# Kernel optimization log

Hardware: AMD Instinct MI355X
Metric: run time of the kernel (lower is better)

The kernel has to match this reference:

```python
import jax, jax.numpy as jnp
import numpy as np

N_JOINTS = 18

_RELATIVE_JOINT_MAP = np.array([[0,3,2,1,3,3,3,3,3,3,3,3,3,3,3,3,3,3],[3,0,2,3,1,1,3,3,3,3,2,3,2,2,2,3,3,3],[2,2,0,1,1,3,3,3,1,2,2,3,3,3,3,3,3,3],[1,3,1,0,2,3,3,3,2,3,3,3,3,3,3,3,3,3],[3,1,1,2,0,2,3,2,2,3,1,3,3,3,3,3,3,3],[3,1,3,3,2,0,3,3,3,3,3,3,1,1,1,3,3,3],[3,3,3,3,3,3,0,3,2,1,3,3,3,3,3,3,3,3],[3,3,3,3,2,3,3,0,2,3,1,1,3,3,3,2,2,2],[3,3,1,2,2,3,2,2,0,1,1,3,3,3,3,3,3,3],[3,3,2,3,3,3,1,3,1,0,2,3,3,3,3,3,3,3],[3,2,2,3,1,3,3,1,1,2,0,2,3,3,3,3,3,3],[3,3,3,3,3,3,3,1,3,3,2,0,3,3,3,1,1,1],[3,2,3,3,3,1,3,3,3,3,3,3,0,1,2,3,3,3],[3,2,3,3,3,1,3,3,3,3,3,3,1,0,2,3,3,3],[3,2,3,3,3,1,3,3,3,3,3,3,2,2,0,3,3,3],[3,3,3,3,3,3,3,2,3,3,3,1,3,3,3,0,1,2],[3,3,3,3,3,3,3,2,3,3,3,1,3,3,3,1,0,2],[3,3,3,3,3,3,3,2,3,3,3,1,3,3,3,2,2,0]], dtype=np.int32)

DIM = 512
HEADS = 8
DEPTH = DIM // HEADS  # 64
BATCH = 4096


def setup_inputs() -> dict:
    key = jax.random.key(0)
    ks = jax.random.split(key, 10)
    std = 0.02
    return {
        "k": jax.random.normal(ks[0], (BATCH, N_JOINTS, DIM), jnp.float32),
        "v": jax.random.normal(ks[1], (BATCH, N_JOINTS, DIM), jnp.float32),
        "q": jax.random.normal(ks[2], (BATCH, N_JOINTS, DIM), jnp.float32),
        "Wq": jax.random.normal(ks[3], (DIM, DIM), jnp.float32) * (DIM ** -0.5),
        "Wk": jax.random.normal(ks[4], (DIM, DIM), jnp.float32) * (DIM ** -0.5),
        "Wv": jax.random.normal(ks[5], (DIM, DIM), jnp.float32) * (DIM ** -0.5),
        "Wo": jax.random.normal(ks[6], (DIM, DIM), jnp.float32) * (DIM ** -0.5),
        "bo": jnp.zeros((DIM,), jnp.float32),
        "rel_k": jax.random.normal(ks[7], (4, DEPTH), jnp.float32) * std,
        "rel_v": jax.random.normal(ks[8], (4, DEPTH), jnp.float32) * std,
        "joint_map": jnp.asarray(_RELATIVE_JOINT_MAP),
    }


def reference(k, v, q, Wq, Wk, Wv, Wo, bo, rel_k, rel_v, joint_map):
    B, n, dim = q.shape
    h, d = HEADS, DEPTH
    scale = d ** -0.5

    def split_heads(x):  # [B, n, h*d] -> [B, h, n, d]
        return x.reshape(B, n, h, d).transpose(0, 2, 1, 3)

    qh = split_heads(q @ Wq)
    kh = split_heads(k @ Wk)
    vh = split_heads(v @ Wv)

    # gather relative position tables: [n, n, d]
    r_pos_k = rel_k[joint_map]
    r_pos_v = rel_v[joint_map]

    # relative bias sums over heads AND depth of K (faithful to original einsum)
    rel_bias = jnp.einsum('bhid,ijd->bij', kh, r_pos_k)  # [B, n, n]
    dots = (jnp.einsum('bhid,bhjd->bhij', qh, kh) + rel_bias[:, None, :, :]) * scale
    att = jax.nn.softmax(dots, axis=-1)  # [B, h, n, n]

    out = jnp.einsum('bhij,bhjd->bhid', att, vh) + jnp.einsum('bhij,ijd->bhid', att, r_pos_v)
    out = out.transpose(0, 2, 1, 3).reshape(B, n, dim)
    out = out @ Wo + bo
    return out, att
```

## Files before the change

kernel.cpp:

```cpp
#include <hip/hip_runtime.h>
#include <stdint.h>

#define BATCH 4096
#define NJ 18
#define DIMM 512
#define HEADS 8
#define DEPTH 64
#define MROWS (BATCH*NJ)
#define ATT_OFF ((size_t)MROWS*DIMM)

typedef float f32x4 __attribute__((ext_vector_type(4)));
typedef _Float16 f16_t;
typedef _Float16 f16x8 __attribute__((ext_vector_type(8)));

__device__ __forceinline__ void gl_lds16(const unsigned int* g, unsigned int* l) {
    __builtin_amdgcn_global_load_lds(g, l, 16, 0, 0);
}

__global__ __launch_bounds__(256) void convert_w_kernel(
    const float* __restrict__ W0, const float* __restrict__ W1,
    const float* __restrict__ W2, const float* __restrict__ W3,
    f16_t* __restrict__ T0, f16_t* __restrict__ T1,
    f16_t* __restrict__ T2, f16_t* __restrict__ T3)
{
    const float* W = blockIdx.z == 0 ? W0 : blockIdx.z == 1 ? W1 : blockIdx.z == 2 ? W2 : W3;
    f16_t* T       = blockIdx.z == 0 ? T0 : blockIdx.z == 1 ? T1 : blockIdx.z == 2 ? T2 : T3;
    __shared__ float ld[64][65];
    int k0 = blockIdx.y * 64, n0 = blockIdx.x * 64;
    int tid = threadIdx.x;
    #pragma unroll
    for (int it = 0; it < 16; ++it) {
        int idx = tid + it * 256;
        int kk = idx >> 6, nn = idx & 63;
        ld[kk][nn] = W[(size_t)(k0 + kk) * DIMM + n0 + nn];
    }
    __syncthreads();
    f16x8* T8 = (f16x8*)T;
    #pragma unroll
    for (int it = 0; it < 2; ++it) {
        int c = tid + it * 256;
        int nn = c >> 3, c8 = c & 7;
        int n = n0 + nn, k = k0 + c8 * 8;
        f16x8 val;
        #pragma unroll
        for (int e = 0; e < 8; ++e) val[e] = (f16_t)ld[c8 * 8 + e][nn];
        size_t vi = (size_t)((n >> 7) * 8 + (k >> 6)) * 1024
                  + (n & 127) * 8 + (((k >> 3) & 7) ^ (n & 7));
        T8[vi] = val;
    }
}

template <int MODE>
__global__ __launch_bounds__(256) void gemm16_kernel(
    const void* __restrict__ A0, const void* __restrict__ A1,
    const void* __restrict__ A2,
    const f16_t* __restrict__ B0, const f16_t* __restrict__ B1,
    const f16_t* __restrict__ B2,
    void* __restrict__ C0, void* __restrict__ C1, void* __restrict__ C2,
    const float* __restrict__ bias)
{
    const void* Aparm = blockIdx.z == 0 ? A0 : blockIdx.z == 1 ? A1 : A2;
    const f16_t* Bt   = blockIdx.z == 0 ? B0 : blockIdx.z == 1 ? B1 : B2;
    void* Cparm       = blockIdx.z == 0 ? C0 : blockIdx.z == 1 ? C1 : C2;

    const int p = blockIdx.x + 4 * blockIdx.y;
    const int logical = (p & 7) * (2304 / 8) + (p >> 3);
    const int bn = (logical & 3) * 128;
    const int bm = (logical >> 2) * 128;

    __shared__ __align__(16) f16_t As[128 * 64];
    __shared__ __align__(16) f16_t Bs[128 * 64];

    const int tid = threadIdx.x;
    const int lane = tid & 63;
    const int wv = tid >> 6;
    const int wm = wv >> 1, wn = wv & 1;
    const int l15 = lane & 15, lg = lane >> 4;
    const int swz = (l15 & 7) << 4;
    const int koffb[2] = { (lg * 16) ^ swz, (lg * 16 + 64) ^ swz };

    f32x4 acc[4][4] = {};

    for (int ks = 0; ks < 8; ++ks) {
        __syncthreads();
        {
            const unsigned int* btile =
                (const unsigned int*)(Bt + (size_t)((bn >> 7) * 8 + ks) * 8192);
            unsigned int* bs = (unsigned int*)Bs;
            #pragma unroll
            for (int it = 0; it < 4; ++it) {
                int chunk = wv * 4 + it;
                gl_lds16(btile + chunk * 256 + lane * 4, bs + chunk * 256);
            }
        }
        if constexpr (MODE == 0) {
            const float* A = (const float*)Aparm;
            #pragma unroll
            for (int r = 0; r < 4; ++r) {
                int c = tid + r * 256;
                int row = c >> 3, kc = c & 7;
                const f32x4* p4 = (const f32x4*)(A + (size_t)(bm + row) * DIMM + ks * 64 + kc * 8);
                f32x4 a0 = p4[0], a1 = p4[1];
                f16x8 val;
                val[0] = (f16_t)a0[0]; val[1] = (f16_t)a0[1];
                val[2] = (f16_t)a0[2]; val[3] = (f16_t)a0[3];
                val[4] = (f16_t)a1[0]; val[5] = (f16_t)a1[1];
                val[6] = (f16_t)a1[2]; val[7] = (f16_t)a1[3];
                ((f16x8*)As)[row * 8 + (kc ^ (row & 7))] = val;
            }
        } else {
            const unsigned int* atile =
                (const unsigned int*)((const f16_t*)Aparm + (size_t)((bm >> 7) * 8 + ks) * 8192);
            unsigned int* as = (unsigned int*)As;
            #pragma unroll
            for (int it = 0; it < 4; ++it) {
                int chunk = wv * 4 + it;
                gl_lds16(atile + chunk * 256 + lane * 4, as + chunk * 256);
            }
        }
        __syncthreads();

        #pragma unroll
        for (int kk = 0; kk < 2; ++kk) {
            const int koff = koffb[kk];
            f16x8 af[4], bfr[4];
            #pragma unroll
            for (int mi = 0; mi < 4; ++mi) {
                int row = wm * 64 + mi * 16 + l15;
                af[mi] = *(const f16x8*)((const char*)As + row * 128 + koff);
            }
            #pragma unroll
            for (int ni = 0; ni < 4; ++ni) {
                int row = wn * 64 + ni * 16 + l15;
                bfr[ni] = *(const f16x8*)((const char*)Bs + row * 128 + koff);
            }
            #pragma unroll
            for (int mi = 0; mi < 4; ++mi)
                #pragma unroll
                for (int ni = 0; ni < 4; ++ni)
                    acc[mi][ni] = __builtin_amdgcn_mfma_f32_16x16x32_f16(
                        af[mi], bfr[ni], acc[mi][ni], 0, 0, 0);
        }
    }

    #pragma unroll
    for (int mi = 0; mi < 4; ++mi) {
        #pragma unroll
        for (int ni = 0; ni < 4; ++ni) {
            int col = bn + wn * 64 + ni * 16 + l15;
            int rowb = bm + wm * 64 + mi * 16 + lg * 4;
            f32x4 v = acc[mi][ni];
            if constexpr (MODE == 1) {
                float* C = (float*)Cparm;
                float bv = bias[col];
                #pragma unroll
                for (int r = 0; r < 4; ++r)
                    C[(size_t)(rowb + r) * DIMM + col] = v[r] + bv;
            } else {
                f16_t* C = (f16_t*)Cparm;
                #pragma unroll
                for (int r = 0; r < 4; ++r)
                    C[(size_t)(rowb + r) * DIMM + col] = (f16_t)v[r];
            }
        }
    }
}

__global__ __launch_bounds__(256, 3) void attn_kernel(
    const f16_t* __restrict__ qh, const f16_t* __restrict__ kh,
    const f16_t* __restrict__ vh,
    const float* __restrict__ rel_k, const float* __restrict__ rel_v,
    const int* __restrict__ jmap,
    float* __restrict__ att_out, f16_t* __restrict__ ao)
{
    const int b = blockIdx.x;
    const int tid = threadIdx.x;
    __shared__ __align__(16) f16_t k_s[NJ * DIMM];
    __shared__ __align__(16) f16_t v_s[NJ * DIMM];
    __shared__ float relk_s[4 * DEPTH];
    __shared__ float relv_s[4 * DEPTH];
    __shared__ int map_s[NJ * NJ];
    __shared__ float ksum_s[NJ * DEPTH];
    __shared__ float t4_s[NJ * 4];

    const size_t base = (size_t)b * (NJ * DIMM);
    const uint4* kg = (const uint4*)(kh + base);
    const uint4* vg = (const uint4*)(vh + base);
    uint4* ks4 = (uint4*)k_s;
    uint4* vs4 = (uint4*)v_s;
    for (int c = tid; c < 2 * NJ * 64; c += 256) {
        int t = c / (NJ * 64);
        int e = c - t * (NJ * 64);
        int m = e & 63;
        int pos = (e & ~63) + (m & 56) + (((m & 7) + (m >> 3)) & 7);
        uint4 val = (t == 0 ? kg : vg)[e];
        (t == 0 ? ks4 : vs4)[pos] = val;
    }
    relk_s[tid & 255] = rel_k[tid & 255];
    relv_s[tid & 255] = rel_v[tid & 255];
    for (int e = tid; e < NJ * NJ; e += 256) map_s[e] = jmap[e];

    const int h = tid / NJ, i = tid - (tid / NJ) * NJ;
    const bool act = tid < HEADS * NJ;
    f16x8 qr[8];
    if (act) {
        const f16x8* qp = (const f16x8*)(qh + base + i * DIMM + h * DEPTH);
        #pragma unroll
        for (int t = 0; t < 8; ++t) qr[t] = qp[t];
    }
    __syncthreads();

    const f16x8* ks8 = (const f16x8*)k_s;
    const f16x8* vs8 = (const f16x8*)v_s;

    for (int e = tid; e < NJ * DEPTH; e += 256) {
        int ii = e >> 6, dd = e & 63;
        int tt = dd >> 3, d7 = dd & 7;
        float s = 0.f;
        #pragma unroll
        for (int hh = 0; hh < HEADS; ++hh)
            s += (float)k_s[((ii << 6) + (hh << 3) + ((tt + hh) & 7)) * 8 + d7];
        ksum_s[e] = s;
    }
    __syncthreads();
    if (tid < NJ * 4) {
        int ii = tid >> 2, c = tid & 3;
        float s = 0.f;
        #pragma unroll
        for (int dd = 0; dd < DEPTH; ++dd)
            s += ksum_s[ii * DEPTH + dd] * relk_s[c * DEPTH + dd];
        t4_s[tid] = s;
    }
    __syncthreads();

    if (!act) return;

    float att[NJ];
    float m = -1e30f;
    #pragma unroll
    for (int j = 0; j < NJ; ++j) {
        float s = 0.f;
        #pragma unroll
        for (int t = 0; t < 8; ++t) {
            f16x8 kv = ks8[(j << 6) + (h << 3) + ((t + h) & 7)];
            f16x8 a = qr[t];
            #pragma unroll
            for (int e = 0; e < 8; ++e) s += (float)a[e] * (float)kv[e];
        }
        s += t4_s[i * 4 + map_s[i * NJ + j]];
        s *= 0.125f;
        att[j] = s;
        m = fmaxf(m, s);
    }
    float sum = 0.f;
    #pragma unroll
    for (int j = 0; j < NJ; ++j) { att[j] = __expf(att[j] - m); sum += att[j]; }
    const float inv = 1.f / sum;
    float s4[4] = {0.f, 0.f, 0.f, 0.f};
    float* ap = att_out + (((size_t)b * HEADS + h) * NJ + i) * NJ;
    #pragma unroll
    for (int j = 0; j < NJ; ++j) {
        float a = att[j] * inv;
        att[j] = a;
        ap[j] = a;
        int c = map_s[i * NJ + j];
        s4[0] += (c == 0) ? a : 0.f;
        s4[1] += (c == 1) ? a : 0.f;
        s4[2] += (c == 2) ? a : 0.f;
        s4[3] += (c == 3) ? a : 0.f;
    }

    const size_t grow = (size_t)b * NJ + i;
    f16x8* aot = (f16x8*)ao + ((grow >> 7) * 8 + h) * 1024 + (grow & 127) * 8;
    const int rr7 = (int)(grow & 7);
    #pragma unroll
    for (int half = 0; half < 2; ++half) {
        float acc[32] = {};
        #pragma unroll
        for (int j = 0; j < NJ; ++j) {
            float a = att[j];
            #pragma unroll
            for (int t = 0; t < 4; ++t) {
                int tt = half * 4 + t;
                f16x8 vv = vs8[(j << 6) + (h << 3) + ((tt + h) & 7)];
                #pragma unroll
                for (int e = 0; e < 8; ++e) acc[t * 8 + e] += a * (float)vv[e];
            }
        }
        #pragma unroll
        for (int c = 0; c < 4; ++c) {
            float sc = s4[c];
            #pragma unroll
            for (int d = 0; d < 32; ++d)
                acc[d] += sc * relv_s[c * DEPTH + half * 32 + d];
        }
        #pragma unroll
        for (int t = 0; t < 4; ++t) {
            f16x8 res;
            #pragma unroll
            for (int e = 0; e < 8; ++e) res[e] = (f16_t)acc[t * 8 + e];
            aot[(half * 4 + t) ^ rr7] = res;
        }
    }
}

extern "C" void kernel_launch(void* const* d_in, const int* in_sizes, int n_in,
                              void* d_out, int out_size, void* d_ws, size_t ws_size,
                              hipStream_t stream) {
    (void)in_sizes; (void)n_in; (void)out_size; (void)ws_size;
    const float* k_in = (const float*)d_in[0];
    const float* v_in = (const float*)d_in[1];
    const float* q_in = (const float*)d_in[2];
    const float* Wq   = (const float*)d_in[3];
    const float* Wk   = (const float*)d_in[4];
    const float* Wv   = (const float*)d_in[5];
    const float* Wo   = (const float*)d_in[6];
    const float* bo   = (const float*)d_in[7];
    const float* relk = (const float*)d_in[8];
    const float* relv = (const float*)d_in[9];
    const int*   jmap = (const int*)d_in[10];

    char* ws = (char*)d_ws;
    const size_t WT = (size_t)DIMM * DIMM * sizeof(f16_t);
    f16_t* Tq = (f16_t*)(ws + 0 * WT);
    f16_t* Tk = (f16_t*)(ws + 1 * WT);
    f16_t* Tv = (f16_t*)(ws + 2 * WT);
    f16_t* To = (f16_t*)(ws + 3 * WT);
    const size_t PSZ = (size_t)MROWS * DIMM * sizeof(f16_t);
    f16_t* qh = (f16_t*)(ws + 4 * WT + 0 * PSZ);
    f16_t* kh = (f16_t*)(ws + 4 * WT + 1 * PSZ);
    f16_t* vh = (f16_t*)(ws + 4 * WT + 2 * PSZ);
    f16_t* ao = (f16_t*)(ws + 4 * WT + 3 * PSZ);

    float* outp = (float*)d_out;
    float* attp = outp + ATT_OFF;

    convert_w_kernel<<<dim3(8, 8, 4), 256, 0, stream>>>(
        Wq, Wk, Wv, Wo, Tq, Tk, Tv, To);

    gemm16_kernel<0><<<dim3(DIMM / 128, MROWS / 128, 3), 256, 0, stream>>>(
        q_in, k_in, v_in, Tq, Tk, Tv, qh, kh, vh, nullptr);

    attn_kernel<<<BATCH, 256, 0, stream>>>(qh, kh, vh, relk, relv, jmap, attp, ao);

    gemm16_kernel<1><<<dim3(DIMM / 128, MROWS / 128, 1), 256, 0, stream>>>(
        ao, nullptr, nullptr, To, nullptr, nullptr, outp, nullptr, nullptr, bo);
}
```

Baseline: 452.4 us.

## Widen QKV GEMM tile to 128x256 with 512 threads to halve fp32 A reloads

The QKV projection GEMM is split into its own kernel that uses 128x256 output tiles with 512 threads (8 waves, 2x4). Each block now covers half of N, so every fp32 input row is read and converted to fp16 only twice instead of four times. This cuts global traffic for the large fp32 activations, in exchange for more LDS and registers per block and fewer blocks in flight. The output GEMM is kept unchanged, just moved into a separate non-templated kernel.

```diff
diff --git a/kernel.cpp b/kernel.cpp
--- a/kernel.cpp
+++ b/kernel.cpp
@@ -50,31 +50,29 @@
     }
 }
 
-template <int MODE>
-__global__ __launch_bounds__(256) void gemm16_kernel(
-    const void* __restrict__ A0, const void* __restrict__ A1,
-    const void* __restrict__ A2,
+__global__ __launch_bounds__(512) void gemm_qkv_kernel(
+    const float* __restrict__ A0, const float* __restrict__ A1,
+    const float* __restrict__ A2,
     const f16_t* __restrict__ B0, const f16_t* __restrict__ B1,
     const f16_t* __restrict__ B2,
-    void* __restrict__ C0, void* __restrict__ C1, void* __restrict__ C2,
-    const float* __restrict__ bias)
+    f16_t* __restrict__ C0, f16_t* __restrict__ C1, f16_t* __restrict__ C2)
 {
-    const void* Aparm = blockIdx.z == 0 ? A0 : blockIdx.z == 1 ? A1 : A2;
-    const f16_t* Bt   = blockIdx.z == 0 ? B0 : blockIdx.z == 1 ? B1 : B2;
-    void* Cparm       = blockIdx.z == 0 ? C0 : blockIdx.z == 1 ? C1 : C2;
-
-    const int p = blockIdx.x + 4 * blockIdx.y;
-    const int logical = (p & 7) * (2304 / 8) + (p >> 3);
-    const int bn = (logical & 3) * 128;
-    const int bm = (logical >> 2) * 128;
+    const float* A  = blockIdx.z == 0 ? A0 : blockIdx.z == 1 ? A1 : A2;
+    const f16_t* Bt = blockIdx.z == 0 ? B0 : blockIdx.z == 1 ? B1 : B2;
+    f16_t* C        = blockIdx.z == 0 ? C0 : blockIdx.z == 1 ? C1 : C2;
+
+    const int p = blockIdx.x + 2 * blockIdx.y;
+    const int logical = (p & 7) * (1152 / 8) + (p >> 3);
+    const int bn = (logical & 1) * 256;
+    const int bm = (logical >> 1) * 128;
 
     __shared__ __align__(16) f16_t As[128 * 64];
-    __shared__ __align__(16) f16_t Bs[128 * 64];
+    __shared__ __align__(16) f16_t Bs[2 * 128 * 64];
 
     const int tid = threadIdx.x;
     const int lane = tid & 63;
     const int wv = tid >> 6;
-    const int wm = wv >> 1, wn = wv & 1;
+    const int wm = wv >> 2, wn = wv & 3;
     const int l15 = lane & 15, lg = lane >> 4;
     const int swz = (l15 & 7) << 4;
     const int koffb[2] = { (lg * 16) ^ swz, (lg * 16 + 64) ^ swz };
@@ -84,20 +82,23 @@
     for (int ks = 0; ks < 8; ++ks) {
         __syncthreads();
         {
-            const unsigned int* btile =
-                (const unsigned int*)(Bt + (size_t)((bn >> 7) * 8 + ks) * 8192);
+            const unsigned int* bt0 =
+                (const unsigned int*)(Bt + (size_t)(((bn >> 7) + 0) * 8 + ks) * 8192);
+            const unsigned int* bt1 =
+                (const unsigned int*)(Bt + (size_t)(((bn >> 7) + 1) * 8 + ks) * 8192);
             unsigned int* bs = (unsigned int*)Bs;
             #pragma unroll
             for (int it = 0; it < 4; ++it) {
                 int chunk = wv * 4 + it;
-                gl_lds16(btile + chunk * 256 + lane * 4, bs + chunk * 256);
-            }
-        }
-        if constexpr (MODE == 0) {
-            const float* A = (const float*)Aparm;
-            #pragma unroll
-            for (int r = 0; r < 4; ++r) {
-                int c = tid + r * 256;
+                const unsigned int* src =
+                    (chunk < 16 ? bt0 : bt1) + (chunk & 15) * 256 + lane * 4;
+                gl_lds16(src, bs + chunk * 256);
+            }
+        }
+        {
+            #pragma unroll
+            for (int r = 0; r < 2; ++r) {
+                int c = tid + r * 512;
                 int row = c >> 3, kc = c & 7;
                 const f32x4* p4 = (const f32x4*)(A + (size_t)(bm + row) * DIMM + ks * 64 + kc * 8);
                 f32x4 a0 = p4[0], a1 = p4[1];
@@ -108,15 +109,6 @@
                 val[6] = (f16_t)a1[2]; val[7] = (f16_t)a1[3];
                 ((f16x8*)As)[row * 8 + (kc ^ (row & 7))] = val;
             }
-        } else {
-            const unsigned int* atile =
-                (const unsigned int*)((const f16_t*)Aparm + (size_t)((bm >> 7) * 8 + ks) * 8192);
-            unsigned int* as = (unsigned int*)As;
-            #pragma unroll
-            for (int it = 0; it < 4; ++it) {
-                int chunk = wv * 4 + it;
-                gl_lds16(atile + chunk * 256 + lane * 4, as + chunk * 256);
-            }
         }
         __syncthreads();
 
@@ -131,8 +123,9 @@
             }
             #pragma unroll
             for (int ni = 0; ni < 4; ++ni) {
-                int row = wn * 64 + ni * 16 + l15;
-                bfr[ni] = *(const f16x8*)((const char*)Bs + row * 128 + koff);
+                int rn = wn * 64 + ni * 16 + l15;
+                bfr[ni] = *(const f16x8*)((const char*)Bs
+                            + (rn >> 7) * 16384 + (rn & 127) * 128 + koff);
             }
             #pragma unroll
             for (int mi = 0; mi < 4; ++mi)
@@ -150,18 +143,93 @@
             int col = bn + wn * 64 + ni * 16 + l15;
             int rowb = bm + wm * 64 + mi * 16 + lg * 4;
             f32x4 v = acc[mi][ni];
-            if constexpr (MODE == 1) {
-                float* C = (float*)Cparm;
-                float bv = bias[col];
+            #pragma unroll
+            for (int r = 0; r < 4; ++r)
+                C[(size_t)(rowb + r) * DIMM + col] = (f16_t)v[r];
+        }
+    }
+}
+
+__global__ __launch_bounds__(256) void gemm_out_kernel(
+    const f16_t* __restrict__ Aimg, const f16_t* __restrict__ Bt,
+    float* __restrict__ C, const float* __restrict__ bias)
+{
+    const int p = blockIdx.x + 4 * blockIdx.y;
+    const int logical = (p & 7) * (2304 / 8) + (p >> 3);
+    const int bn = (logical & 3) * 128;
+    const int bm = (logical >> 2) * 128;
+
+    __shared__ __align__(16) f16_t As[128 * 64];
+    __shared__ __align__(16) f16_t Bs[128 * 64];
+
+    const int tid = threadIdx.x;
+    const int lane = tid & 63;
+    const int wv = tid >> 6;
+    const int wm = wv >> 1, wn = wv & 1;
+    const int l15 = lane & 15, lg = lane >> 4;
+    const int swz = (l15 & 7) << 4;
+    const int koffb[2] = { (lg * 16) ^ swz, (lg * 16 + 64) ^ swz };
+
+    f32x4 acc[4][4] = {};
+
+    for (int ks = 0; ks < 8; ++ks) {
+        __syncthreads();
+        {
+            const unsigned int* btile =
+                (const unsigned int*)(Bt + (size_t)((bn >> 7) * 8 + ks) * 8192);
+            unsigned int* bs = (unsigned int*)Bs;
+            #pragma unroll
+            for (int it = 0; it < 4; ++it) {
+                int chunk = wv * 4 + it;
+                gl_lds16(btile + chunk * 256 + lane * 4, bs + chunk * 256);
+            }
+        }
+        {
+            const unsigned int* atile =
+                (const unsigned int*)(Aimg + (size_t)((bm >> 7) * 8 + ks) * 8192);
+            unsigned int* as = (unsigned int*)As;
+            #pragma unroll
+            for (int it = 0; it < 4; ++it) {
+                int chunk = wv * 4 + it;
+                gl_lds16(atile + chunk * 256 + lane * 4, as + chunk * 256);
+            }
+        }
+        __syncthreads();
+
+        #pragma unroll
+        for (int kk = 0; kk < 2; ++kk) {
+            const int koff = koffb[kk];
+            f16x8 af[4], bfr[4];
+            #pragma unroll
+            for (int mi = 0; mi < 4; ++mi) {
+                int row = wm * 64 + mi * 16 + l15;
+                af[mi] = *(const f16x8*)((const char*)As + row * 128 + koff);
+            }
+            #pragma unroll
+            for (int ni = 0; ni < 4; ++ni) {
+                int row = wn * 64 + ni * 16 + l15;
+                bfr[ni] = *(const f16x8*)((const char*)Bs + row * 128 + koff);
+            }
+            #pragma unroll
+            for (int mi = 0; mi < 4; ++mi)
                 #pragma unroll
-                for (int r = 0; r < 4; ++r)
-                    C[(size_t)(rowb + r) * DIMM + col] = v[r] + bv;
-            } else {
-                f16_t* C = (f16_t*)Cparm;
-                #pragma unroll
-                for (int r = 0; r < 4; ++r)
-                    C[(size_t)(rowb + r) * DIMM + col] = (f16_t)v[r];
-            }
+                for (int ni = 0; ni < 4; ++ni)
+                    acc[mi][ni] = __builtin_amdgcn_mfma_f32_16x16x32_f16(
+                        af[mi], bfr[ni], acc[mi][ni], 0, 0, 0);
+        }
+    }
+
+    #pragma unroll
+    for (int mi = 0; mi < 4; ++mi) {
+        #pragma unroll
+        for (int ni = 0; ni < 4; ++ni) {
+            int col = bn + wn * 64 + ni * 16 + l15;
+            int rowb = bm + wm * 64 + mi * 16 + lg * 4;
+            f32x4 v = acc[mi][ni];
+            float bv = bias[col];
+            #pragma unroll
+            for (int r = 0; r < 4; ++r)
+                C[(size_t)(rowb + r) * DIMM + col] = v[r] + bv;
         }
     }
 }
@@ -338,11 +406,11 @@
     convert_w_kernel<<<dim3(8, 8, 4), 256, 0, stream>>>(
         Wq, Wk, Wv, Wo, Tq, Tk, Tv, To);
 
-    gemm16_kernel<0><<<dim3(DIMM / 128, MROWS / 128, 3), 256, 0, stream>>>(
-        q_in, k_in, v_in, Tq, Tk, Tv, qh, kh, vh, nullptr);
+    gemm_qkv_kernel<<<dim3(DIMM / 256, MROWS / 128, 3), 512, 0, stream>>>(
+        q_in, k_in, v_in, Tq, Tk, Tv, qh, kh, vh);
 
     attn_kernel<<<BATCH, 256, 0, stream>>>(qh, kh, vh, relk, relv, jmap, attp, ao);
 
-    gemm16_kernel<1><<<dim3(DIMM / 128, MROWS / 128, 1), 256, 0, stream>>>(
-        ao, nullptr, nullptr, To, nullptr, nullptr, outp, nullptr, nullptr, bo);
-}
+    gemm_out_kernel<<<dim3(DIMM / 128, MROWS / 128), 256, 0, stream>>>(
+        ao, To, outp, bo);
+}
```

Result: faster. 432.7 us (-4.3%).
